# Optimization experiments

Hardware: AMD Instinct MI355X
Metric: run time of the kernel (lower is better)

Reference implementation:

```python
import jax, jax.numpy as jnp
import numpy as np

B, N, D, H, L = 16, 1024, 256, 128, 2  # batch, nodes, feat dim, gcn_hidden, n_layers (D == 2*H)


def setup_inputs() -> dict:
    key = jax.random.key(0)
    ks = jax.random.split(key, 16)
    inp = {
        "gcn_input": jax.random.normal(ks[0], (B, N, D), jnp.float32),
        # scale adjacencies by 1/N so aggregated features stay O(1)
        "latent_adj": jax.random.uniform(ks[1], (B, N, N), jnp.float32) / N,
        "dep_adj": jax.random.uniform(ks[2], (B, N, N), jnp.float32) / N,
        # stacked per-layer parameters (leading dim L); layers share shapes since D == 2*H
        "refine_gate": jax.random.normal(ks[3], (L, D, 1), jnp.float32) * 0.02,
        "gate_W_in": jax.random.normal(ks[4], (L, D, 1), jnp.float32) * 0.02,
        "gate_b_in": jnp.zeros((L, 1), jnp.float32),
        "gate_W_out": jax.random.normal(ks[5], (L, D, 1), jnp.float32) * 0.02,
        "gate_b_out": jnp.zeros((L, 1), jnp.float32),
        "fc_in_W": jax.random.normal(ks[6], (L, H, D), jnp.float32) * 0.02,
        "fc_in_b": jnp.zeros((L, H), jnp.float32),
        "fc_out_W": jax.random.normal(ks[7], (L, H, D), jnp.float32) * 0.02,
        "fc_out_b": jnp.zeros((L, H), jnp.float32),
        "ln_g": jnp.ones((L, 2 * H), jnp.float32),
        "ln_b": jnp.zeros((L, 2 * H), jnp.float32),
    }
    return inp


def _gcn_layer(x, latent, dep, rg, Wgi, bgi, Wgo, bgo, Wi, bi, Wo, bo, g, b):
    # refine gate blends dependency and latent adjacency per source node
    gate = jax.nn.sigmoid(x @ rg)  # [B,N,1]
    A_in = gate * dep + (1.0 - gate) * latent  # [B,N,N]
    A_out = gate * jnp.swapaxes(dep, -1, -2) + (1.0 - gate) * jnp.swapaxes(latent, -1, -2)
    Ax_in = A_in @ x   # [B,N,D]
    Ax_out = A_out @ x
    # gcn gates (scalar bias added after the gated product, as in torch)
    Ax_in = Ax_in * jax.nn.sigmoid(Ax_in @ Wgi) + bgi
    Ax_out = Ax_out * jax.nn.sigmoid(Ax_out @ Wgo) + bgo
    # rec_fc(Ax) + rec_fc(x): weight applied to sum, bias counted twice (faithful)
    h_in = (Ax_in + x) @ Wi.T + 2.0 * bi   # [B,N,H]
    h_out = (Ax_out + x) @ Wo.T + 2.0 * bo
    h = jnp.concatenate([h_in, h_out], axis=-1)  # [B,N,2H]
    mu = jnp.mean(h, axis=-1, keepdims=True)
    var = jnp.var(h, axis=-1, keepdims=True)
    h = (h - mu) * jax.lax.rsqrt(var + 1e-5) * g + b
    return jax.nn.gelu(h, approximate=False)


def reference(gcn_input, latent_adj, dep_adj, refine_gate, gate_W_in, gate_b_in,
              gate_W_out, gate_b_out, fc_in_W, fc_in_b, fc_out_W, fc_out_b, ln_g, ln_b):
    x = gcn_input
    for l in range(refine_gate.shape[0]):  # small fixed layer count
        x = _gcn_layer(x, latent_adj, dep_adj, refine_gate[l],
                       gate_W_in[l], gate_b_in[l], gate_W_out[l], gate_b_out[l],
                       fc_in_W[l], fc_in_b[l], fc_out_W[l], fc_out_b[l],
                       ln_g[l], ln_b[l])
    return x
```

## Files before the change

### kernel.cpp

```cpp
#include <hip/hip_runtime.h>
#include <hip/hip_bf16.h>
#include <cstdint>

#define B_ 16
#define N_ 1024
#define D_ 256
#define H_ 128

typedef unsigned short u16;
typedef __attribute__((ext_vector_type(8))) short bf16x8;
typedef __attribute__((ext_vector_type(4))) float f32x4;

__device__ __forceinline__ u16 f2bf(float f) {
    union { float f; uint32_t u; } v; v.f = f;
    return (u16)((v.u + 0x7FFFu + ((v.u >> 16) & 1u)) >> 16);
}
__device__ __forceinline__ float bf2f(u16 h) {
    union { uint32_t u; float f; } v; v.u = ((uint32_t)h) << 16;
    return v.f;
}

typedef __attribute__((address_space(3))) void lds_void;
typedef const __attribute__((address_space(1))) void g_void;

__device__ __forceinline__ void gl_lds16(const void* g, void* l) {
    __builtin_amdgcn_global_load_lds((g_void*)g, (lds_void*)l, 16, 0, 0);
}

__device__ __forceinline__ void vm_wait4() { asm volatile("s_waitcnt vmcnt(4)" ::: "memory"); }
__device__ __forceinline__ void vm_wait3() { asm volatile("s_waitcnt vmcnt(3)" ::: "memory"); }
__device__ __forceinline__ void vm_wait2() { asm volatile("s_waitcnt vmcnt(2)" ::: "memory"); }
__device__ __forceinline__ void vm_wait0() { asm volatile("s_waitcnt vmcnt(0)" ::: "memory"); }
__device__ __forceinline__ void lgkm0()   { asm volatile("s_waitcnt lgkmcnt(0)" ::: "memory"); }
__device__ __forceinline__ void schedb()  { __builtin_amdgcn_sched_barrier(0); }

__global__ __launch_bounds__(256) void k_conv_adj(
    const float* __restrict__ dep, const float* __restrict__ lat,
    u16* __restrict__ depb, u16* __restrict__ latb,
    u16* __restrict__ depTb, u16* __restrict__ latTb)
{
    __shared__ u16 tile[64][64];
    const int bz = blockIdx.z;
    const int b = bz >> 1;
    const float* src = (bz & 1) ? lat : dep;
    u16* dstN = (bz & 1) ? latb : depb;
    u16* dstT = (bz & 1) ? latTb : depTb;
    const int r0 = blockIdx.y * 64, c0 = blockIdx.x * 64;
    const int t = threadIdx.x;
    const int r = t >> 2, cg = (t & 3) * 16;

    const float* srow = src + ((size_t)b * N_ + r0 + r) * N_ + c0 + cg;
    bf16x8 lo, hi;
    {
        const float4 v0 = *(const float4*)(srow);
        const float4 v1 = *(const float4*)(srow + 4);
        const float4 v2 = *(const float4*)(srow + 8);
        const float4 v3 = *(const float4*)(srow + 12);
        lo[0] = (short)f2bf(v0.x); lo[1] = (short)f2bf(v0.y); lo[2] = (short)f2bf(v0.z); lo[3] = (short)f2bf(v0.w);
        lo[4] = (short)f2bf(v1.x); lo[5] = (short)f2bf(v1.y); lo[6] = (short)f2bf(v1.z); lo[7] = (short)f2bf(v1.w);
        hi[0] = (short)f2bf(v2.x); hi[1] = (short)f2bf(v2.y); hi[2] = (short)f2bf(v2.z); hi[3] = (short)f2bf(v2.w);
        hi[4] = (short)f2bf(v3.x); hi[5] = (short)f2bf(v3.y); hi[6] = (short)f2bf(v3.z); hi[7] = (short)f2bf(v3.w);
    }
    u16* nrow = dstN + ((size_t)b * N_ + r0 + r) * N_ + c0 + cg;
    *(bf16x8*)nrow = lo;
    *(bf16x8*)(nrow + 8) = hi;

    const int g0 = (t & 3) * 2;
    const int s = (r & 7) ^ ((r >> 3) & 7);
    *(bf16x8*)(&tile[r][((g0    ) ^ s) * 8]) = lo;
    *(bf16x8*)(&tile[r][((g0 + 1) ^ s) * 8]) = hi;
    __syncthreads();

    const int sc = t >> 2, rg2 = (t & 3) * 16;
    bf16x8 o0, o1;
    #pragma unroll
    for (int i = 0; i < 8; ++i) {
        const int R = rg2 + i;
        const int sR = (R & 7) ^ ((R >> 3) & 7);
        o0[i] = (short)tile[R][(((sc >> 3) ^ sR) * 8) + (sc & 7)];
    }
    #pragma unroll
    for (int i = 0; i < 8; ++i) {
        const int R = rg2 + 8 + i;
        const int sR = (R & 7) ^ ((R >> 3) & 7);
        o1[i] = (short)tile[R][(((sc >> 3) ^ sR) * 8) + (sc & 7)];
    }
    u16* dT = dstT + ((size_t)b * N_ + c0 + sc) * N_ + r0 + rg2;
    *(bf16x8*)dT = o0;
    *(bf16x8*)(dT + 8) = o1;
}

__global__ __launch_bounds__(256) void k_gate_xt(
    const float* __restrict__ x, const float* __restrict__ rg,
    float* __restrict__ gate, u16* __restrict__ xT,
    const float* __restrict__ wi, const float* __restrict__ wo,
    u16* __restrict__ wib, u16* __restrict__ wob)
{
    if (blockIdx.y >= B_) {
        const int i = ((blockIdx.y - B_) * 32 + blockIdx.x) * 256 + threadIdx.x;
        wib[i] = f2bf(wi[i]);
        wob[i] = f2bf(wo[i]);
        return;
    }

    __shared__ u16 lx[D_][36];
    __shared__ float srg[D_];
    const int b = blockIdx.y, n0 = blockIdx.x * 32;
    const int t = threadIdx.x;
    srg[t] = rg[t];
    __syncthreads();

    const int r = t >> 3, cg = t & 7;
    const float* xrow = x + ((size_t)b * N_ + n0 + r) * D_;
    float dot = 0.f;
    #pragma unroll
    for (int u = 0; u < 8; ++u) {
        const int c = cg * 32 + u * 4;
        const float4 v = *(const float4*)(xrow + c);
        lx[c][r] = f2bf(v.x); lx[c + 1][r] = f2bf(v.y);
        lx[c + 2][r] = f2bf(v.z); lx[c + 3][r] = f2bf(v.w);
        dot += v.x * srg[c] + v.y * srg[c + 1] + v.z * srg[c + 2] + v.w * srg[c + 3];
    }
    dot += __shfl_down(dot, 4, 8);
    dot += __shfl_down(dot, 2, 8);
    dot += __shfl_down(dot, 1, 8);
    if (cg == 0) gate[(size_t)b * N_ + n0 + r] = 1.f / (1.f + expf(-dot));
    __syncthreads();

    #pragma unroll
    for (int i = 0; i < 8; ++i) {
        const int unit = i * 256 + t;
        const int d = unit >> 3, nch = (unit & 7) * 4;
        ushort4 wv;
        wv.x = lx[d][nch];     wv.y = lx[d][nch + 1];
        wv.z = lx[d][nch + 2]; wv.w = lx[d][nch + 3];
        *(ushort4*)(xT + ((size_t)b * D_ + d) * N_ + n0 + nch) = wv;
    }
}

__global__ __launch_bounds__(512, 2) void k_gemm_ax(
    const u16* __restrict__ depb, const u16* __restrict__ latb,
    const u16* __restrict__ depTb, const u16* __restrict__ latTb,
    const u16* __restrict__ xT,
    const float* __restrict__ gate,
    const float* __restrict__ Wgi, const float* __restrict__ Wgo,
    const float* __restrict__ bgi, const float* __restrict__ bgo,
    const float* __restrict__ xcur,
    u16* __restrict__ axin, u16* __restrict__ axout)
{
    __shared__ __align__(16) char smem[51712];
    u16* const sb = (u16*)smem;
    float* hbuf = (float*)smem;
    float* psum = (float*)(smem + 49152);
    float* sh_s = (float*)(smem + 51200);

    const int bid = blockIdx.x;
    const int logical = (bid & 7) * 32 + (bid >> 3);
    const int b = logical >> 4;
    const int rem = logical & 15;
    const int z = rem >> 3;
    const int m0 = (rem & 7) * 128;

    const u16* A1 = z ? depTb : depb;
    const u16* A2 = z ? latTb : latb;
    const float* Wg = z ? Wgo : Wgi;
    const float bg0 = z ? bgo[0] : bgi[0];
    u16* outp = z ? axout : axin;

    const int t = threadIdx.x;
    const int lane = t & 63;
    const int w = t >> 6;
    const int wr = w >> 2, wc = w & 3;

    const int arow = t >> 2;
    const int akq = t & 3;
    const float gv = gate[(size_t)b * N_ + m0 + arow];
    const u16* gA1 = A1 + ((size_t)b * N_ + m0 + arow) * N_ + akq * 8;
    const u16* gA2 = A2 + ((size_t)b * N_ + m0 + arow) * N_ + akq * 8;
    const int awoff = arow * 32 + ((akq ^ ((arow >> 1) & 3)) << 3);

    const int rl = lane >> 2;
    const int kk = (((lane & 3) ^ ((lane >> 3) & 3)) << 3);
    const u16* gB0 = xT + ((size_t)b * D_ + (w * 2) * 16 + rl) * N_ + kk;
    const u16* gB1 = xT + ((size_t)b * D_ + (w * 2 + 1) * 16 + rl) * N_ + kk;
    const int boff0 = 4096 + (w * 2) * 512;
    const int boff1 = 4096 + (w * 2 + 1) * 512;

    const int mrow = lane & 15;
    const int hi = lane >> 4;
    const int kg = (((lane >> 4) ^ ((mrow >> 1) & 3)) << 3);

    f32x4 acc[4][4];
    const f32x4 fz = {0.f, 0.f, 0.f, 0.f};
    #pragma unroll
    for (int i = 0; i < 4; ++i)
        #pragma unroll
        for (int j = 0; j < 4; ++j) acc[i][j] = fz;

    bf16x8 rA1x, rA2x, rA1y, rA2y;

    auto blend_store = [&](const bf16x8& a1v, const bf16x8& a2v, u16* dst) {
        bf16x8 bl;
        #pragma unroll
        for (int u = 0; u < 8; ++u) {
            const float f1 = bf2f((u16)a1v[u]);
            const float f2 = bf2f((u16)a2v[u]);
            bl[u] = (short)f2bf(f2 + gv * (f1 - f2));
        }
        *(bf16x8*)dst = bl;
    };

    rA1x = *(const bf16x8*)(gA1);       rA2x = *(const bf16x8*)(gA2);
    blend_store(rA1x, rA2x, sb + awoff);
    rA1x = *(const bf16x8*)(gA1 + 32);  rA2x = *(const bf16x8*)(gA2 + 32);
    gl_lds16(gB0, sb + boff0);          gl_lds16(gB1, sb + boff1);
    blend_store(rA1x, rA2x, sb + 12288 + awoff);
    rA1x = *(const bf16x8*)(gA1 + 64);  rA2x = *(const bf16x8*)(gA2 + 64);
    gl_lds16(gB0 + 32, sb + 12288 + boff0); gl_lds16(gB1 + 32, sb + 12288 + boff1);
    vm_wait2();
    lgkm0();
    schedb(); __builtin_amdgcn_s_barrier(); schedb();

    auto body = [&](int ks, bf16x8& c1, bf16x8& c2, bf16x8& n1, bf16x8& n2) {
        if (ks <= 28) {
            n1 = *(const bf16x8*)(gA1 + (ks + 3) * 32);
            n2 = *(const bf16x8*)(gA2 + (ks + 3) * 32);
        }
        const u16* sA = sb + (ks & 1) * 12288;
        const u16* sBc = sA + 4096;
        bf16x8 a[4], fbv[4];
        #pragma unroll
        for (int mt = 0; mt < 4; ++mt)
            a[mt] = *(const bf16x8*)(sA + (wr * 64 + mt * 16 + mrow) * 32 + kg);
        #pragma unroll
        for (int nt = 0; nt < 4; ++nt)
            fbv[nt] = *(const bf16x8*)(sBc + (wc * 64 + nt * 16 + mrow) * 32 + kg);
        #pragma unroll
        for (int mt = 0; mt < 4; ++mt)
            #pragma unroll
            for (int nt = 0; nt < 4; ++nt)
                acc[mt][nt] = __builtin_amdgcn_mfma_f32_16x16x32_bf16(a[mt], fbv[nt], acc[mt][nt], 0, 0, 0);
        schedb();
        __builtin_amdgcn_s_barrier();
        schedb();
        if (ks <= 29) {
            u16* cb = sb + (ks & 1) * 12288;
            blend_store(c1, c2, cb + awoff);
            gl_lds16(gB0 + (ks + 2) * 32, cb + boff0);
            gl_lds16(gB1 + (ks + 2) * 32, cb + boff1);
        }
        if (ks <= 28) vm_wait4();
        else if (ks == 29) vm_wait2();
        else if (ks == 30) vm_wait0();
        lgkm0();
        schedb();
        __builtin_amdgcn_s_barrier();
        schedb();
    };

    for (int kp = 0; kp < 16; ++kp) {
        body(2 * kp,     rA1x, rA2x, rA1y, rA2y);
        body(2 * kp + 1, rA1y, rA2y, rA1x, rA2x);
    }
    __syncthreads();

    float wgv[4];
    #pragma unroll
    for (int nt = 0; nt < 4; ++nt) wgv[nt] = Wg[wc * 64 + nt * 16 + mrow];
    #pragma unroll
    for (int mt = 0; mt < 4; ++mt) {
        #pragma unroll
        for (int rr = 0; rr < 4; ++rr) {
            float p = acc[mt][0][rr] * wgv[0] + acc[mt][1][rr] * wgv[1]
                    + acc[mt][2][rr] * wgv[2] + acc[mt][3][rr] * wgv[3];
            p += __shfl_xor(p, 1, 16);
            p += __shfl_xor(p, 2, 16);
            p += __shfl_xor(p, 4, 16);
            p += __shfl_xor(p, 8, 16);
            if (mrow == 0) psum[(wr * 64 + mt * 16 + hi * 4 + rr) * 4 + wc] = p;
        }
    }
    __syncthreads();
    if (t < 128) {
        const float d = psum[t * 4] + psum[t * 4 + 1] + psum[t * 4 + 2] + psum[t * 4 + 3];
        sh_s[t] = 1.f / (1.f + expf(-d));
    }
    __syncthreads();

    #pragma unroll
    for (int p = 0; p < 4; ++p) {
        if (wr == (p >> 1)) {
            #pragma unroll
            for (int mtl = 0; mtl < 2; ++mtl) {
                const int mt = (p & 1) * 2 + mtl;
                #pragma unroll
                for (int nt = 0; nt < 4; ++nt) {
                    const int col = wc * 64 + nt * 16 + mrow;
                    #pragma unroll
                    for (int rr = 0; rr < 4; ++rr) {
                        const int hrow = mtl * 16 + hi * 4 + rr;
                        hbuf[hrow * 260 + col] = acc[mt][nt][rr];
                    }
                }
            }
        }
        __syncthreads();
        {
            const int sr = t >> 4;
            const int sc0 = (t & 15) * 16;
            const int grow = p * 32 + sr;
            const float s = sh_s[grow];
            const size_t gb = ((size_t)b * N_ + m0 + grow) * D_ + sc0;
            const float* xr = xcur + gb;
            u16* orow = outp + gb;
            bf16x8 o0, o1;
            #pragma unroll
            for (int u = 0; u < 8; ++u)
                o0[u] = (short)f2bf(hbuf[sr * 260 + sc0 + u] * s + bg0 + xr[u]);
            #pragma unroll
            for (int u = 0; u < 8; ++u)
                o1[u] = (short)f2bf(hbuf[sr * 260 + sc0 + 8 + u] * s + bg0 + xr[8 + u]);
            *(bf16x8*)orow = o0;
            *(bf16x8*)(orow + 8) = o1;
        }
        __syncthreads();
    }
}

__global__ __launch_bounds__(512, 2) void k_fc_ln(
    const u16* __restrict__ axin, const u16* __restrict__ axout,
    const u16* __restrict__ Wib, const u16* __restrict__ Wob,
    const float* __restrict__ bi, const float* __restrict__ bo,
    const float* __restrict__ lg, const float* __restrict__ lb,
    float* __restrict__ outp)
{
    __shared__ __align__(16) char smem[51712];
    u16* const sb = (u16*)smem;
    float* hbuf = (float*)smem;
    float* psum = (float*)(smem + 49152);
    float* sh_mu = (float*)(smem + 51200);
    float* sh_rs = (float*)(smem + 51456);

    const int bid = blockIdx.x;
    const int logical = (bid & 7) * 32 + (bid >> 3);
    const int b = logical >> 4;
    const int m0 = (logical & 15) * 64;

    const int t = threadIdx.x, lane = t & 63, w = t >> 6;
    const int wr = w >> 2, wc = w & 3;
    const int half = wc >> 1;

    const int rl = lane >> 2;
    const int kk = (((lane & 3) ^ ((lane >> 3) & 3)) << 3);

    const u16* gsrc[3];
    int loff[3];
    #pragma unroll
    for (int ci = 0; ci < 3; ++ci) {
        const int c = w * 3 + ci;
        if (c < 4) {
            gsrc[ci] = axin + ((size_t)b * N_ + m0 + c * 16 + rl) * D_ + kk;
            loff[ci] = c * 512;
        } else if (c < 8) {
            gsrc[ci] = axout + ((size_t)b * N_ + m0 + (c - 4) * 16 + rl) * D_ + kk;
            loff[ci] = 2048 + (c - 4) * 512;
        } else {
            const int cw = c - 8;
            const u16* base = (cw < 8) ? (Wib + (size_t)(cw * 16 + rl) * D_)
                                       : (Wob + (size_t)((cw - 8) * 16 + rl) * D_);
            gsrc[ci] = base + kk;
            loff[ci] = 4096 + cw * 512;
        }
    }

    f32x4 acc[2][4];
    const f32x4 fz = {0.f, 0.f, 0.f, 0.f};
    #pragma unroll
    for (int i = 0; i < 2; ++i)
        #pragma unroll
        for (int j = 0; j < 4; ++j) acc[i][j] = fz;

    #pragma unroll
    for (int ci = 0; ci < 3; ++ci) gl_lds16(gsrc[ci], sb + loff[ci]);
    #pragma unroll
    for (int ci = 0; ci < 3; ++ci) gl_lds16(gsrc[ci] + 32, sb + 12288 + loff[ci]);
    vm_wait3();
    lgkm0();
    schedb(); __builtin_amdgcn_s_barrier(); schedb();

    const int mrow = lane & 15;
    const int hi = lane >> 4;
    const int kg = (((lane >> 4) ^ ((mrow >> 1) & 3)) << 3);

    for (int ks = 0; ks < 8; ++ks) {
        const u16* cur = sb + (ks & 1) * 12288;
        const u16* sA = cur + (half ? 2048 : 0);
        const u16* sW = cur + 4096;
        bf16x8 a[2], fbv[4];
        #pragma unroll
        for (int mt = 0; mt < 2; ++mt)
            a[mt] = *(const bf16x8*)(sA + (wr * 32 + mt * 16 + mrow) * 32 + kg);
        #pragma unroll
        for (int nt = 0; nt < 4; ++nt)
            fbv[nt] = *(const bf16x8*)(sW + (wc * 64 + nt * 16 + mrow) * 32 + kg);
        #pragma unroll
        for (int mt = 0; mt < 2; ++mt)
            #pragma unroll
            for (int nt = 0; nt < 4; ++nt)
                acc[mt][nt] = __builtin_amdgcn_mfma_f32_16x16x32_bf16(a[mt], fbv[nt], acc[mt][nt], 0, 0, 0);
        schedb();
        __builtin_amdgcn_s_barrier();
        schedb();
        if (ks <= 5) {
            u16* nb = sb + (ks & 1) * 12288;
            #pragma unroll
            for (int ci = 0; ci < 3; ++ci) gl_lds16(gsrc[ci] + (ks + 2) * 32, nb + loff[ci]);
        }
        if (ks <= 5) vm_wait3();
        else if (ks == 6) vm_wait0();
        lgkm0();
        schedb();
        __builtin_amdgcn_s_barrier();
        schedb();
    }
    __syncthreads();

    float bc[4];
    #pragma unroll
    for (int nt = 0; nt < 4; ++nt) {
        const int colh = wc * 64 + nt * 16 + mrow;
        bc[nt] = 2.f * (colh < 128 ? bi[colh] : bo[colh - 128]);
    }
    #pragma unroll
    for (int mt = 0; mt < 2; ++mt)
        #pragma unroll
        for (int rr = 0; rr < 4; ++rr) {
            const int lrow = wr * 32 + mt * 16 + hi * 4 + rr;
            float s = 0.f, ss = 0.f;
            #pragma unroll
            for (int nt = 0; nt < 4; ++nt) {
                const float v = acc[mt][nt][rr] + bc[nt];
                s += v; ss += v * v;
            }
            s += __shfl_xor(s, 1, 16);  ss += __shfl_xor(ss, 1, 16);
            s += __shfl_xor(s, 2, 16);  ss += __shfl_xor(ss, 2, 16);
            s += __shfl_xor(s, 4, 16);  ss += __shfl_xor(ss, 4, 16);
            s += __shfl_xor(s, 8, 16);  ss += __shfl_xor(ss, 8, 16);
            if (mrow == 0) {
                psum[lrow * 8 + wc * 2] = s;
                psum[lrow * 8 + wc * 2 + 1] = ss;
            }
        }
    __syncthreads();
    if (t < 64) {
        const float s = psum[t * 8] + psum[t * 8 + 2] + psum[t * 8 + 4] + psum[t * 8 + 6];
        const float ss = psum[t * 8 + 1] + psum[t * 8 + 3] + psum[t * 8 + 5] + psum[t * 8 + 7];
        const float mu = s * (1.f / 256.f);
        const float var = ss * (1.f / 256.f) - mu * mu;
        sh_mu[t] = mu;
        sh_rs[t] = rsqrtf(var + 1e-5f);
    }
    __syncthreads();

    #pragma unroll
    for (int p = 0; p < 2; ++p) {
        if (wr == p) {
            #pragma unroll
            for (int mt = 0; mt < 2; ++mt)
                #pragma unroll
                for (int nt = 0; nt < 4; ++nt) {
                    const int col = wc * 64 + nt * 16 + mrow;
                    #pragma unroll
                    for (int rr = 0; rr < 4; ++rr) {
                        const int hrow = mt * 16 + hi * 4 + rr;
                        hbuf[hrow * 260 + col] = acc[mt][nt][rr] + bc[nt];
                    }
                }
        }
        __syncthreads();
        {
            const int sr = t >> 4;
            const int sc0 = (t & 15) * 16;
            const int grow = p * 32 + sr;
            const float mu = sh_mu[grow], rs = sh_rs[grow];
            float* orow = outp + ((size_t)b * N_ + m0 + grow) * D_ + sc0;
            #pragma unroll
            for (int q = 0; q < 4; ++q) {
                const float4 gg = *(const float4*)(lg + sc0 + q * 4);
                const float4 bb = *(const float4*)(lb + sc0 + q * 4);
                float4 o;
                const float v0 = (hbuf[sr * 260 + sc0 + q * 4    ] - mu) * rs * gg.x + bb.x;
                const float v1 = (hbuf[sr * 260 + sc0 + q * 4 + 1] - mu) * rs * gg.y + bb.y;
                const float v2 = (hbuf[sr * 260 + sc0 + q * 4 + 2] - mu) * rs * gg.z + bb.z;
                const float v3 = (hbuf[sr * 260 + sc0 + q * 4 + 3] - mu) * rs * gg.w + bb.w;
                o.x = 0.5f * v0 * (1.f + erff(v0 * 0.70710678118654752f));
                o.y = 0.5f * v1 * (1.f + erff(v1 * 0.70710678118654752f));
                o.z = 0.5f * v2 * (1.f + erff(v2 * 0.70710678118654752f));
                o.w = 0.5f * v3 * (1.f + erff(v3 * 0.70710678118654752f));
                *(float4*)(orow + q * 4) = o;
            }
        }
        __syncthreads();
    }
}

extern "C" void kernel_launch(void* const* d_in, const int* in_sizes, int n_in,
                              void* d_out, int out_size, void* d_ws, size_t ws_size,
                              hipStream_t stream)
{
    (void)in_sizes; (void)n_in; (void)out_size; (void)ws_size;

    const float* x0  = (const float*)d_in[0];
    const float* lat = (const float*)d_in[1];
    const float* dep = (const float*)d_in[2];
    const float* rg  = (const float*)d_in[3];
    const float* Wgi = (const float*)d_in[4];
    const float* bgi = (const float*)d_in[5];
    const float* Wgo = (const float*)d_in[6];
    const float* bgo = (const float*)d_in[7];
    const float* fiW = (const float*)d_in[8];
    const float* fib = (const float*)d_in[9];
    const float* foW = (const float*)d_in[10];
    const float* fob = (const float*)d_in[11];
    const float* lng = (const float*)d_in[12];
    const float* lnb = (const float*)d_in[13];

    char* ws = (char*)d_ws;
    size_t off = 0;
    auto alloc = [&](size_t bytes) {
        char* p = ws + off;
        off += (bytes + 255) & ~(size_t)255;
        return p;
    };
    u16* depb  = (u16*)alloc(2ull * B_ * N_ * N_);
    u16* latb  = (u16*)alloc(2ull * B_ * N_ * N_);
    u16* depTb = (u16*)alloc(2ull * B_ * N_ * N_);
    u16* latTb = (u16*)alloc(2ull * B_ * N_ * N_);
    u16* xT    = (u16*)alloc(2ull * B_ * D_ * N_);
    u16* axin  = (u16*)alloc(2ull * B_ * N_ * D_);
    u16* axout = (u16*)alloc(2ull * B_ * N_ * D_);
    float* gate = (float*)alloc(4ull * B_ * N_);
    float* xbuf = (float*)alloc(4ull * B_ * N_ * D_);
    u16* Wib = (u16*)alloc(2ull * H_ * D_);
    u16* Wob = (u16*)alloc(2ull * H_ * D_);

    k_conv_adj<<<dim3(16, 16, 32), 256, 0, stream>>>(dep, lat, depb, latb, depTb, latTb);

    const float* xcur = x0;
    for (int l = 0; l < 2; ++l) {
        k_gate_xt<<<dim3(32, B_ + 4), 256, 0, stream>>>(
            xcur, rg + l * D_, gate, xT,
            fiW + (size_t)l * H_ * D_, foW + (size_t)l * H_ * D_, Wib, Wob);
        k_gemm_ax<<<dim3(256), 512, 0, stream>>>(
            depb, latb, depTb, latTb, xT, gate,
            Wgi + l * D_, Wgo + l * D_, bgi + l, bgo + l,
            xcur, axin, axout);
        const bool last = (l == 1);
        k_fc_ln<<<dim3(256), 512, 0, stream>>>(
            axin, axout, Wib, Wob,
            fib + l * H_, fob + l * H_,
            lng + l * 2 * H_, lnb + l * 2 * H_,
            last ? (float*)d_out : xbuf);
        xcur = xbuf;
    }
}
```

Baseline: 323.2 us.

## Retile adjacency GEMM to 64-row blocks with 256 threads and 512 blocks

Changes k_gemm_ax from 128x256 tiles with 8 waves to 64x256 tiles with 4 waves, doubling the grid to 512 blocks. Each wave now loads four B chunks per k-step, so the vmcnt waits are adjusted. Shared memory per block shrinks. The goal is better occupancy and load balance across CUs, at the cost of re-reading the xT B-operand twice as often relative to the A work.

Result: slower. 344.6 us (+6.6%).

```diff
diff --git a/kernel.cpp b/kernel.cpp
--- a/kernel.cpp
+++ b/kernel.cpp
@@ -27,9 +27,9 @@
     __builtin_amdgcn_global_load_lds((g_void*)g, (lds_void*)l, 16, 0, 0);
 }
 
+__device__ __forceinline__ void vm_wait6() { asm volatile("s_waitcnt vmcnt(6)" ::: "memory"); }
 __device__ __forceinline__ void vm_wait4() { asm volatile("s_waitcnt vmcnt(4)" ::: "memory"); }
 __device__ __forceinline__ void vm_wait3() { asm volatile("s_waitcnt vmcnt(3)" ::: "memory"); }
-__device__ __forceinline__ void vm_wait2() { asm volatile("s_waitcnt vmcnt(2)" ::: "memory"); }
 __device__ __forceinline__ void vm_wait0() { asm volatile("s_waitcnt vmcnt(0)" ::: "memory"); }
 __device__ __forceinline__ void lgkm0()   { asm volatile("s_waitcnt lgkmcnt(0)" ::: "memory"); }
 __device__ __forceinline__ void schedb()  { __builtin_amdgcn_sched_barrier(0); }
@@ -138,7 +138,7 @@
     }
 }
 
-__global__ __launch_bounds__(512, 2) void k_gemm_ax(
+__global__ __launch_bounds__(256, 2) void k_gemm_ax(
     const u16* __restrict__ depb, const u16* __restrict__ latb,
     const u16* __restrict__ depTb, const u16* __restrict__ latTb,
     const u16* __restrict__ xT,
@@ -148,18 +148,18 @@
     const float* __restrict__ xcur,
     u16* __restrict__ axin, u16* __restrict__ axout)
 {
-    __shared__ __align__(16) char smem[51712];
+    __shared__ __align__(16) char smem[42240];
     u16* const sb = (u16*)smem;
     float* hbuf = (float*)smem;
-    float* psum = (float*)(smem + 49152);
-    float* sh_s = (float*)(smem + 51200);
+    float* psum = (float*)(smem + 40960);
+    float* sh_s = (float*)(smem + 41984);
 
     const int bid = blockIdx.x;
-    const int logical = (bid & 7) * 32 + (bid >> 3);
-    const int b = logical >> 4;
-    const int rem = logical & 15;
-    const int z = rem >> 3;
-    const int m0 = (rem & 7) * 128;
+    const int logical = (bid & 7) * 64 + (bid >> 3);
+    const int b = logical >> 5;
+    const int rem = logical & 31;
+    const int z = rem >> 4;
+    const int m0 = (rem & 15) * 64;
 
     const u16* A1 = z ? depTb : depb;
     const u16* A2 = z ? latTb : latb;
@@ -170,7 +170,6 @@
     const int t = threadIdx.x;
     const int lane = t & 63;
     const int w = t >> 6;
-    const int wr = w >> 2, wc = w & 3;
 
     const int arow = t >> 2;
     const int akq = t & 3;
@@ -181,10 +180,14 @@
 
     const int rl = lane >> 2;
     const int kk = (((lane & 3) ^ ((lane >> 3) & 3)) << 3);
-    const u16* gB0 = xT + ((size_t)b * D_ + (w * 2) * 16 + rl) * N_ + kk;
-    const u16* gB1 = xT + ((size_t)b * D_ + (w * 2 + 1) * 16 + rl) * N_ + kk;
-    const int boff0 = 4096 + (w * 2) * 512;
-    const int boff1 = 4096 + (w * 2 + 1) * 512;
+    const u16* gB[4];
+    int boff[4];
+    #pragma unroll
+    for (int j = 0; j < 4; ++j) {
+        const int ch = w * 4 + j;
+        gB[j] = xT + ((size_t)b * D_ + ch * 16 + rl) * N_ + kk;
+        boff[j] = 2048 + ch * 512;
+    }
 
     const int mrow = lane & 15;
     const int hi = lane >> 4;
@@ -213,11 +216,13 @@
     rA1x = *(const bf16x8*)(gA1);       rA2x = *(const bf16x8*)(gA2);
     blend_store(rA1x, rA2x, sb + awoff);
     rA1x = *(const bf16x8*)(gA1 + 32);  rA2x = *(const bf16x8*)(gA2 + 32);
-    gl_lds16(gB0, sb + boff0);          gl_lds16(gB1, sb + boff1);
-    blend_store(rA1x, rA2x, sb + 12288 + awoff);
+    blend_store(rA1x, rA2x, sb + 10240 + awoff);
+    #pragma unroll
+    for (int j = 0; j < 4; ++j) gl_lds16(gB[j], sb + boff[j]);
     rA1x = *(const bf16x8*)(gA1 + 64);  rA2x = *(const bf16x8*)(gA2 + 64);
-    gl_lds16(gB0 + 32, sb + 12288 + boff0); gl_lds16(gB1 + 32, sb + 12288 + boff1);
-    vm_wait2();
+    #pragma unroll
+    for (int j = 0; j < 4; ++j) gl_lds16(gB[j] + 32, sb + 10240 + boff[j]);
+    vm_wait6();
     lgkm0();
     schedb(); __builtin_amdgcn_s_barrier(); schedb();
 
@@ -226,15 +231,16 @@
             n1 = *(const bf16x8*)(gA1 + (ks + 3) * 32);
             n2 = *(const bf16x8*)(gA2 + (ks + 3) * 32);
         }
-        const u16* sA = sb + (ks & 1) * 12288;
-        const u16* sBc = sA + 4096;
+        schedb();
+        const u16* sA = sb + (ks & 1) * 10240;
+        const u16* sBc = sA + 2048;
         bf16x8 a[4], fbv[4];
         #pragma unroll
         for (int mt = 0; mt < 4; ++mt)
-            a[mt] = *(const bf16x8*)(sA + (wr * 64 + mt * 16 + mrow) * 32 + kg);
+            a[mt] = *(const bf16x8*)(sA + (mt * 16 + mrow) * 32 + kg);
         #pragma unroll
         for (int nt = 0; nt < 4; ++nt)
-            fbv[nt] = *(const bf16x8*)(sBc + (wc * 64 + nt * 16 + mrow) * 32 + kg);
+            fbv[nt] = *(const bf16x8*)(sBc + (w * 64 + nt * 16 + mrow) * 32 + kg);
         #pragma unroll
         for (int mt = 0; mt < 4; ++mt)
             #pragma unroll
@@ -244,13 +250,13 @@
         __builtin_amdgcn_s_barrier();
         schedb();
         if (ks <= 29) {
-            u16* cb = sb + (ks & 1) * 12288;
+            u16* cb = sb + (ks & 1) * 10240;
             blend_store(c1, c2, cb + awoff);
-            gl_lds16(gB0 + (ks + 2) * 32, cb + boff0);
-            gl_lds16(gB1 + (ks + 2) * 32, cb + boff1);
-        }
-        if (ks <= 28) vm_wait4();
-        else if (ks == 29) vm_wait2();
+            #pragma unroll
+            for (int j = 0; j < 4; ++j) gl_lds16(gB[j] + (ks + 2) * 32, cb + boff[j]);
+        }
+        if (ks <= 28) vm_wait6();
+        else if (ks == 29) vm_wait4();
         else if (ks == 30) vm_wait0();
         lgkm0();
         schedb();
@@ -266,7 +272,7 @@
 
     float wgv[4];
     #pragma unroll
-    for (int nt = 0; nt < 4; ++nt) wgv[nt] = Wg[wc * 64 + nt * 16 + mrow];
+    for (int nt = 0; nt < 4; ++nt) wgv[nt] = Wg[w * 64 + nt * 16 + mrow];
     #pragma unroll
     for (int mt = 0; mt < 4; ++mt) {
         #pragma unroll
@@ -277,51 +283,56 @@
             p += __shfl_xor(p, 2, 16);
             p += __shfl_xor(p, 4, 16);
             p += __shfl_xor(p, 8, 16);
-            if (mrow == 0) psum[(wr * 64 + mt * 16 + hi * 4 + rr) * 4 + wc] = p;
-        }
-    }
-    __syncthreads();
-    if (t < 128) {
+            if (mrow == 0) psum[(mt * 16 + hi * 4 + rr) * 4 + w] = p;
+        }
+    }
+    __syncthreads();
+    if (t < 64) {
         const float d = psum[t * 4] + psum[t * 4 + 1] + psum[t * 4 + 2] + psum[t * 4 + 3];
         sh_s[t] = 1.f / (1.f + expf(-d));
     }
     __syncthreads();
 
     #pragma unroll
-    for (int p = 0; p < 4; ++p) {
-        if (wr == (p >> 1)) {
-            #pragma unroll
-            for (int mtl = 0; mtl < 2; ++mtl) {
-                const int mt = (p & 1) * 2 + mtl;
+    for (int p = 0; p < 2; ++p) {
+        #pragma unroll
+        for (int mtl = 0; mtl < 2; ++mtl) {
+            const int mt = p * 2 + mtl;
+            #pragma unroll
+            for (int nt = 0; nt < 4; ++nt) {
+                const int col = w * 64 + nt * 16 + mrow;
                 #pragma unroll
-                for (int nt = 0; nt < 4; ++nt) {
-                    const int col = wc * 64 + nt * 16 + mrow;
-                    #pragma unroll
-                    for (int rr = 0; rr < 4; ++rr) {
-                        const int hrow = mtl * 16 + hi * 4 + rr;
-                        hbuf[hrow * 260 + col] = acc[mt][nt][rr];
-                    }
+                for (int rr = 0; rr < 4; ++rr) {
+                    const int hrow = mtl * 16 + hi * 4 + rr;
+                    hbuf[hrow * 260 + col] = acc[mt][nt][rr];
                 }
             }
         }
         __syncthreads();
         {
-            const int sr = t >> 4;
-            const int sc0 = (t & 15) * 16;
-            const int grow = p * 32 + sr;
-            const float s = sh_s[grow];
-            const size_t gb = ((size_t)b * N_ + m0 + grow) * D_ + sc0;
+            const int sr = t >> 3;
+            const int c0 = (t & 7) * 32;
+            const float s = sh_s[p * 32 + sr];
+            const size_t gb = ((size_t)b * N_ + m0 + p * 32 + sr) * D_ + c0;
             const float* xr = xcur + gb;
             u16* orow = outp + gb;
-            bf16x8 o0, o1;
+            bf16x8 o0, o1, o2, o3;
             #pragma unroll
             for (int u = 0; u < 8; ++u)
-                o0[u] = (short)f2bf(hbuf[sr * 260 + sc0 + u] * s + bg0 + xr[u]);
+                o0[u] = (short)f2bf(hbuf[sr * 260 + c0 + u] * s + bg0 + xr[u]);
             #pragma unroll
             for (int u = 0; u < 8; ++u)
-                o1[u] = (short)f2bf(hbuf[sr * 260 + sc0 + 8 + u] * s + bg0 + xr[8 + u]);
+                o1[u] = (short)f2bf(hbuf[sr * 260 + c0 + 8 + u] * s + bg0 + xr[8 + u]);
+            #pragma unroll
+            for (int u = 0; u < 8; ++u)
+                o2[u] = (short)f2bf(hbuf[sr * 260 + c0 + 16 + u] * s + bg0 + xr[16 + u]);
+            #pragma unroll
+            for (int u = 0; u < 8; ++u)
+                o3[u] = (short)f2bf(hbuf[sr * 260 + c0 + 24 + u] * s + bg0 + xr[24 + u]);
             *(bf16x8*)orow = o0;
             *(bf16x8*)(orow + 8) = o1;
+            *(bf16x8*)(orow + 16) = o2;
+            *(bf16x8*)(orow + 24) = o3;
         }
         __syncthreads();
     }
@@ -551,7 +562,7 @@
         k_gate_xt<<<dim3(32, B_ + 4), 256, 0, stream>>>(
             xcur, rg + l * D_, gate, xT,
             fiW + (size_t)l * H_ * D_, foW + (size_t)l * H_ * D_, Wib, Wob);
-        k_gemm_ax<<<dim3(256), 512, 0, stream>>>(
+        k_gemm_ax<<<dim3(512), 256, 0, stream>>>(
             depb, latb, depTb, latTb, xT, gate,
             Wgi + l * D_, Wgo + l * D_, bgi + l, bgo + l,
             xcur, axin, axout);
```

## Fuse next-layer gate and x transpose into LayerNorm epilogue

Applied to the files above, without the earlier changes.

The first layer's fc+LayerNorm kernel now computes the next layer's refine-gate dot product and writes the bf16 transposed x directly from its LDS tile. The second k_gate_xt launch is removed, and the weight conversion for both layers is hoisted into a single initial launch with extra blocks. This cuts one kernel launch and one full re-read of x. In exchange, the epilogue gains extra LDS writes, shuffles and a barrier. The modified k_gate_xt grid (B_+8) assumes that kernel's hidden body handles both layers' weights, which cannot be verified here.

Result: no change. 320.8 us (-0.7%).

```diff
diff --git a/kernel.cpp b/kernel.cpp
--- a/kernel.cpp
+++ b/kernel.cpp
@@ -327,12 +327,15 @@
     }
 }
 
+template<int FUSE>
 __global__ __launch_bounds__(512, 2) void k_fc_ln(
     const u16* __restrict__ axin, const u16* __restrict__ axout,
     const u16* __restrict__ Wib, const u16* __restrict__ Wob,
     const float* __restrict__ bi, const float* __restrict__ bo,
     const float* __restrict__ lg, const float* __restrict__ lb,
-    float* __restrict__ outp)
+    float* __restrict__ outp,
+    const float* __restrict__ rgN, float* __restrict__ gateN,
+    u16* __restrict__ xTN)
 {
     __shared__ __align__(16) char smem[51712];
     u16* const sb = (u16*)smem;
@@ -484,6 +487,7 @@
             const int grow = p * 32 + sr;
             const float mu = sh_mu[grow], rs = sh_rs[grow];
             float* orow = outp + ((size_t)b * N_ + m0 + grow) * D_ + sc0;
+            float gdot = 0.f;
             #pragma unroll
             for (int q = 0; q < 4; ++q) {
                 const float4 gg = *(const float4*)(lg + sc0 + q * 4);
@@ -498,9 +502,40 @@
                 o.z = 0.5f * v2 * (1.f + erff(v2 * 0.70710678118654752f));
                 o.w = 0.5f * v3 * (1.f + erff(v3 * 0.70710678118654752f));
                 *(float4*)(orow + q * 4) = o;
+                if (FUSE) {
+                    hbuf[sr * 260 + sc0 + q * 4    ] = o.x;
+                    hbuf[sr * 260 + sc0 + q * 4 + 1] = o.y;
+                    hbuf[sr * 260 + sc0 + q * 4 + 2] = o.z;
+                    hbuf[sr * 260 + sc0 + q * 4 + 3] = o.w;
+                    const float4 rv = *(const float4*)(rgN + sc0 + q * 4);
+                    gdot += o.x * rv.x + o.y * rv.y + o.z * rv.z + o.w * rv.w;
+                }
             }
+            if (FUSE) {
+                gdot += __shfl_xor(gdot, 1, 16);
+                gdot += __shfl_xor(gdot, 2, 16);
+                gdot += __shfl_xor(gdot, 4, 16);
+                gdot += __shfl_xor(gdot, 8, 16);
+                if ((t & 15) == 0)
+                    gateN[(size_t)b * N_ + m0 + grow] = 1.f / (1.f + expf(-gdot));
+            }
         }
         __syncthreads();
+        if (FUSE) {
+            const int d = t >> 1;
+            const int nh = (t & 1) * 16;
+            bf16x8 y0, y1;
+            #pragma unroll
+            for (int i = 0; i < 8; ++i)
+                y0[i] = (short)f2bf(hbuf[(nh + i) * 260 + d]);
+            #pragma unroll
+            for (int i = 0; i < 8; ++i)
+                y1[i] = (short)f2bf(hbuf[(nh + 8 + i) * 260 + d]);
+            u16* xrow = xTN + ((size_t)b * D_ + d) * N_ + m0 + p * 32 + nh;
+            *(bf16x8*)xrow = y0;
+            *(bf16x8*)(xrow + 8) = y1;
+            __syncthreads();
+        }
     }
 }
 
@@ -541,26 +576,26 @@
     u16* axout = (u16*)alloc(2ull * B_ * N_ * D_);
     float* gate = (float*)alloc(4ull * B_ * N_);
     float* xbuf = (float*)alloc(4ull * B_ * N_ * D_);
-    u16* Wib = (u16*)alloc(2ull * H_ * D_);
-    u16* Wob = (u16*)alloc(2ull * H_ * D_);
+    u16* Wib = (u16*)alloc(2ull * 2 * H_ * D_);
+    u16* Wob = (u16*)alloc(2ull * 2 * H_ * D_);
 
     k_conv_adj<<<dim3(16, 16, 32), 256, 0, stream>>>(dep, lat, depb, latb, depTb, latTb);
 
-    const float* xcur = x0;
-    for (int l = 0; l < 2; ++l) {
-        k_gate_xt<<<dim3(32, B_ + 4), 256, 0, stream>>>(
-            xcur, rg + l * D_, gate, xT,
-            fiW + (size_t)l * H_ * D_, foW + (size_t)l * H_ * D_, Wib, Wob);
-        k_gemm_ax<<<dim3(256), 512, 0, stream>>>(
-            depb, latb, depTb, latTb, xT, gate,
-            Wgi + l * D_, Wgo + l * D_, bgi + l, bgo + l,
-            xcur, axin, axout);
-        const bool last = (l == 1);
-        k_fc_ln<<<dim3(256), 512, 0, stream>>>(
-            axin, axout, Wib, Wob,
-            fib + l * H_, fob + l * H_,
-            lng + l * 2 * H_, lnb + l * 2 * H_,
-            last ? (float*)d_out : xbuf);
-        xcur = xbuf;
-    }
-}
+    k_gate_xt<<<dim3(32, B_ + 8), 256, 0, stream>>>(
+        x0, rg, gate, xT, fiW, foW, Wib, Wob);
+
+    k_gemm_ax<<<dim3(256), 512, 0, stream>>>(
+        depb, latb, depTb, latTb, xT, gate,
+        Wgi, Wgo, bgi, bgo, x0, axin, axout);
+    k_fc_ln<1><<<dim3(256), 512, 0, stream>>>(
+        axin, axout, Wib, Wob, fib, fob, lng, lnb,
+        xbuf, rg + D_, gate, xT);
+
+    k_gemm_ax<<<dim3(256), 512, 0, stream>>>(
+        depb, latb, depTb, latTb, xT, gate,
+        Wgi + D_, Wgo + D_, bgi + 1, bgo + 1, xbuf, axin, axout);
+    k_fc_ln<0><<<dim3(256), 512, 0, stream>>>(
+        axin, axout, Wib + (size_t)H_ * D_, Wob + (size_t)H_ * D_,
+        fib + H_, fob + H_, lng + 2 * H_, lnb + 2 * H_,
+        (float*)d_out, nullptr, nullptr, nullptr);
+}
```
